# Optimization experiments

Hardware: AMD Instinct MI355X
Metric: run time of the kernel (lower is better)

Reference implementation:

```python
import jax, jax.numpy as jnp
import numpy as np

B, S, H, NH = 4, 1024, 4096, 32
QL, KVL, RD, ND, VD = 1536, 512, 64, 128, 128  # q_lora, kv_lora, rope, nope, v head dims
QHD = ND + RD  # 192
EPS = 1e-6


def setup_inputs() -> dict:
    key = jax.random.key(0)
    ks = jax.random.split(key, 10)
    def w(k, fan_in, fan_out):
        return jax.random.normal(k, (fan_in, fan_out), jnp.float32) * (fan_in ** -0.5)
    return {
        "hidden_states": jax.random.normal(ks[0], (B, S, H), jnp.float32),
        "cos": jax.random.uniform(ks[1], (S, RD), jnp.float32),
        "sin": jax.random.uniform(ks[2], (S, RD), jnp.float32),
        "position_ids": jax.random.randint(ks[3], (B, S), 0, S, jnp.int64 if jax.config.jax_enable_x64 else jnp.int32),
        "Wqa": w(ks[4], H, QL),
        "gqa": jnp.ones((QL,), jnp.float32),
        "bqa": jnp.zeros((QL,), jnp.float32),
        "Wqb": w(ks[5], QL, NH * QHD),
        "Wkva": w(ks[6], H, KVL + RD),
        "gkva": jnp.ones((KVL,), jnp.float32),
        "bkva": jnp.zeros((KVL,), jnp.float32),
        "Wkvb": w(ks[7], KVL, NH * (ND + VD)),
        "Wo": w(ks[8], NH * VD, H),
    }


def _ln(x, g, b):
    m = jnp.mean(x, -1, keepdims=True)
    v = jnp.mean(jnp.square(x - m), -1, keepdims=True)
    return (x - m) * jax.lax.rsqrt(v + EPS) * g + b


def _rotate_half(x):
    x1, x2 = jnp.split(x, 2, axis=-1)
    return jnp.concatenate([-x2, x1], axis=-1)


def _rope(t, cos_g, sin_g):
    # t: (B,S,h,RD); cos_g/sin_g: (B,S,1,RD)
    return t * cos_g + _rotate_half(t) * sin_g


def reference(hidden_states, cos, sin, position_ids, Wqa, gqa, bqa, Wqb, Wkva, gkva, bkva, Wkvb, Wo):
    hs = hidden_states
    # low-rank Q path: q_a_proj -> LN -> q_b_proj
    q = _ln(hs @ Wqa, gqa, bqa) @ Wqb                      # (B,S,NH*QHD)
    q = q.reshape(B, S, NH, QHD)
    q_nope, q_pe = q[..., :ND], q[..., ND:]                # (B,S,NH,128/64)
    # compressed KV + MQA rope key
    ckv = hs @ Wkva                                        # (B,S,KVL+RD)
    kv_c, k_pe = ckv[..., :KVL], ckv[..., KVL:]
    kv_cn = _ln(kv_c, gkva, bkva)                          # (B,S,512)
    # partial-dim RoPE on rope slices only
    cos_g = cos[position_ids][:, :, None, :]               # (B,S,1,RD)
    sin_g = sin[position_ids][:, :, None, :]
    q_pe = _rope(q_pe, cos_g, sin_g)                       # (B,S,NH,RD)
    k_pe = _rope(k_pe[:, :, None, :], cos_g, sin_g)        # (B,S,1,RD)
    # decompress latent into per-head k_nope and v
    kv = (kv_cn @ Wkvb).reshape(B, S, NH, ND + VD)
    k_nope, v = kv[..., :ND], kv[..., ND:]
    k = jnp.concatenate([k_nope, jnp.broadcast_to(k_pe, (B, S, NH, RD))], axis=-1)  # (B,S,NH,192)
    qs = jnp.concatenate([q_nope, q_pe], axis=-1)          # (B,S,NH,192)
    # causal attention
    scores = jnp.einsum('bqhd,bkhd->bhqk', qs, k) * (QHD ** -0.5)
    causal = jnp.tril(jnp.ones((S, S), bool))
    scores = jnp.where(causal, scores, jnp.finfo(scores.dtype).min)
    p = jax.nn.softmax(scores, axis=-1)                    # (B,NH,S,S)
    o = jnp.einsum('bhqk,bkhd->bqhd', p, v).reshape(B, S, NH * VD)
    return o @ Wo                                          # (B,S,H)
```

## Files before the change

kernel.cpp:

```cpp
#include <hip/hip_runtime.h>

#define B_ 4
#define S_ 1024
#define H_ 4096
#define NH_ 32
#define QHD_ 192
#define EPS_ 1e-6f

typedef __bf16 bf16x8 __attribute__((ext_vector_type(8)));
typedef float floatx4 __attribute__((ext_vector_type(4)));

__device__ __forceinline__ unsigned short f2bf(float f) {
  unsigned int u = __builtin_bit_cast(unsigned int, f);
  u += 0x7fffu + ((u >> 16) & 1u);
  return (unsigned short)(u >> 16);
}
__device__ __forceinline__ float bf2f(unsigned short s) {
  return __builtin_bit_cast(float, ((unsigned int)s) << 16);
}

__device__ __forceinline__ void gload16(const unsigned short* g, unsigned short* l) {
  __builtin_amdgcn_global_load_lds(
      (const __attribute__((address_space(1))) void*)g,
      (__attribute__((address_space(3))) void*)l, 16, 0, 0);
}

__global__ __launch_bounds__(256) void convert_kernel(
    const float* __restrict__ x, unsigned short* __restrict__ y)
{
  const int i = (blockIdx.x * 256 + threadIdx.x) * 8;
  const float4 a = *(const float4*)(x + i);
  const float4 b = *(const float4*)(x + i + 4);
  ushort4 u, v;
  u.x = f2bf(a.x); u.y = f2bf(a.y); u.z = f2bf(a.z); u.w = f2bf(a.w);
  v.x = f2bf(b.x); v.y = f2bf(b.y); v.z = f2bf(b.z); v.w = f2bf(b.w);
  *(ushort4*)(y + i) = u;
  *(ushort4*)(y + i + 4) = v;
}

__global__ __launch_bounds__(256) void transpose_kernel(
    const float* __restrict__ W, unsigned short* __restrict__ Wt,
    const int K, const int N)
{
  __shared__ float tile[32][33];
  const int tx = threadIdx.x & 31, ty = threadIdx.x >> 5;
  const int nb = blockIdx.x << 5, kb = blockIdx.y << 5;
#pragma unroll
  for (int j = 0; j < 4; ++j)
    tile[ty + j * 8][tx] = W[(size_t)(kb + ty + j * 8) * N + nb + tx];
  __syncthreads();
#pragma unroll
  for (int j = 0; j < 4; ++j)
    Wt[(size_t)(nb + ty + j * 8) * K + kb + tx] = f2bf(tile[tx][ty + j * 8]);
}

template<int OMODE>
__global__ __launch_bounds__(256, 2) void gemm_bt(
    const unsigned short* __restrict__ A, const unsigned short* __restrict__ Bt,
    void* __restrict__ Cv, const int N, const int K,
    const int lda, const int ldb, const int ldc)
{
  __shared__ unsigned short As[128 * 32];
  __shared__ unsigned short Bs[128 * 32];

  const int t = threadIdx.x;
  const int m0 = blockIdx.x * 128, n0 = blockIdx.y * 128;
  const int w = t >> 6, lane = t & 63;
  const int wm = (w >> 1) << 6, wn = (w & 1) << 6;
  const int lm = lane & 15, lq = lane >> 4;

  const floatx4 vzero = {0.f, 0.f, 0.f, 0.f};
  floatx4 acc[4][4];
#pragma unroll
  for (int i = 0; i < 4; ++i)
#pragma unroll
    for (int j = 0; j < 4; ++j) acc[i][j] = vzero;

  const int srow = (w << 5) + (lane >> 2);
  const int skc = (lane & 3) << 3;
  const unsigned short* gA = A + (size_t)(m0 + srow) * lda + skc;
  const unsigned short* gB = Bt + (size_t)(n0 + srow) * ldb + skc;
  unsigned short* lA0 = &As[(w << 1) * 512];
  unsigned short* lA1 = &As[((w << 1) + 1) * 512];
  unsigned short* lB0 = &Bs[(w << 1) * 512];
  unsigned short* lB1 = &Bs[((w << 1) + 1) * 512];

  const int nk = K >> 5;
  for (int kb = 0; kb < nk; ++kb) {
    const int k0 = kb << 5;
    __syncthreads();
    gload16(gA + k0, lA0);
    gload16(gA + (size_t)16 * lda + k0, lA1);
    gload16(gB + k0, lB0);
    gload16(gB + (size_t)16 * ldb + k0, lB1);
    __syncthreads();

    bf16x8 af[4], bfr[4];
#pragma unroll
    for (int mi = 0; mi < 4; ++mi)
      af[mi] = *(const bf16x8*)&As[(wm + mi * 16 + lm) * 32 + (lq << 3)];
#pragma unroll
    for (int ni = 0; ni < 4; ++ni)
      bfr[ni] = *(const bf16x8*)&Bs[(wn + ni * 16 + lm) * 32 + (lq << 3)];
#pragma unroll
    for (int mi = 0; mi < 4; ++mi)
#pragma unroll
      for (int ni = 0; ni < 4; ++ni)
        acc[mi][ni] = __builtin_amdgcn_mfma_f32_16x16x32_bf16(af[mi], bfr[ni], acc[mi][ni], 0, 0, 0);
  }

#pragma unroll
  for (int mi = 0; mi < 4; ++mi) {
    const int row = m0 + wm + mi * 16 + (lq << 2);
#pragma unroll
    for (int ni = 0; ni < 4; ++ni) {
      const int col = n0 + wn + ni * 16 + lm;
      if (col < N) {
#pragma unroll
        for (int r = 0; r < 4; ++r) {
          if constexpr (OMODE == 0)
            ((float*)Cv)[(size_t)(row + r) * ldc + col] = acc[mi][ni][r];
          else if constexpr (OMODE == 1)
            ((unsigned short*)Cv)[(size_t)(row + r) * ldc + col] = f2bf(acc[mi][ni][r]);
          else {
            const int rr2 = row + r;
            ((unsigned short*)Cv)[(((size_t)(rr2 >> 10) * NH_ + (col >> 8)) * S_ + (rr2 & 1023)) * 256 + (col & 255)] = f2bf(acc[mi][ni][r]);
          }
        }
      }
    }
  }
}

__global__ __launch_bounds__(256) void ln_kernel(
    const float* __restrict__ x, const float* __restrict__ g,
    const float* __restrict__ bias, unsigned short* __restrict__ y,
    const int L, const int xstride, const int ystride)
{
  __shared__ float sh[4];
  const int t = threadIdx.x;
  const float* xr = x + (size_t)blockIdx.x * xstride;
  unsigned short* yr = y + (size_t)blockIdx.x * ystride;
  const int n = L >> 8;
  float vals[6];
  float s = 0.f;
  for (int i = 0; i < n; ++i) { vals[i] = xr[t + (i << 8)]; s += vals[i]; }
#pragma unroll
  for (int off = 32; off; off >>= 1) s += __shfl_down(s, off);
  if ((t & 63) == 0) sh[t >> 6] = s;
  __syncthreads();
  const float mean = (sh[0] + sh[1] + sh[2] + sh[3]) / (float)L;
  float vs = 0.f;
  for (int i = 0; i < n; ++i) { const float d = vals[i] - mean; vs += d * d; }
#pragma unroll
  for (int off = 32; off; off >>= 1) vs += __shfl_down(vs, off);
  __syncthreads();
  if ((t & 63) == 0) sh[t >> 6] = vs;
  __syncthreads();
  const float inv = rsqrtf((sh[0] + sh[1] + sh[2] + sh[3]) / (float)L + EPS_);
  for (int i = 0; i < n; ++i) {
    const int c = t + (i << 8);
    yr[c] = f2bf((vals[i] - mean) * inv * g[c] + bias[c]);
  }
}

__global__ __launch_bounds__(256) void rope_q_kernel(
    unsigned short* __restrict__ q, const float* __restrict__ cosp,
    const float* __restrict__ sinp, const int* __restrict__ pos)
{
  const int i = blockIdx.x * 256 + threadIdx.x;
  const int p = i & 31;
  const int h = (i >> 5) & 31;
  const int bs = i >> 10;
  const int pid = pos[bs];
  const size_t base = ((size_t)bs * NH_ + h) * QHD_ + 128;
  const float x1 = bf2f(q[base + p]);
  const float x2 = bf2f(q[base + p + 32]);
  const float* cr = cosp + (size_t)pid * 64;
  const float* sr = sinp + (size_t)pid * 64;
  q[base + p]      = f2bf(x1 * cr[p] - x2 * sr[p]);
  q[base + p + 32] = f2bf(x2 * cr[p + 32] + x1 * sr[p + 32]);
}

__global__ __launch_bounds__(256) void rope_k_kernel(
    const float* __restrict__ ckv, const float* __restrict__ cosp,
    const float* __restrict__ sinp, const int* __restrict__ pos,
    unsigned short* __restrict__ kpe)
{
  const int i = blockIdx.x * 256 + threadIdx.x;
  const int p = i & 31;
  const int bs = i >> 5;
  const int pid = pos[bs];
  const float* row = ckv + (size_t)bs * 576 + 512;
  const float x1 = row[p], x2 = row[p + 32];
  const float* cr = cosp + (size_t)pid * 64;
  const float* sr = sinp + (size_t)pid * 64;
  kpe[(size_t)bs * 64 + p]      = f2bf(x1 * cr[p] - x2 * sr[p]);
  kpe[(size_t)bs * 64 + p + 32] = f2bf(x2 * cr[p + 32] + x1 * sr[p + 32]);
}

__global__ __launch_bounds__(256, 3) void attn_kernel(
    const unsigned short* __restrict__ qb, const unsigned short* __restrict__ kvb,
    const unsigned short* __restrict__ kpe, unsigned short* __restrict__ o)
{
  __shared__ unsigned short Ks[64 * 200];
  __shared__ unsigned short Vt[128 * 72];
  __shared__ unsigned short Ps[4 * 16 * 72];

  const int t = threadIdx.x;
  const int qt = (int)gridDim.x - 1 - (int)blockIdx.x;
  const int h = blockIdx.y, b = blockIdx.z;
  const int w = t >> 6, lane = t & 63;
  const int lm = lane & 15, lq = lane >> 4;
  const float SCALE2 = 0.10411754645f;

  const unsigned short* qp = qb + (((size_t)b * S_ + (qt << 6) + (w << 4) + lm) * NH_ + h) * QHD_;
  bf16x8 qf[6];
#pragma unroll
  for (int s = 0; s < 6; ++s) qf[s] = *(const bf16x8*)(qp + s * 32 + (lq << 3));

  const floatx4 vzero = {0.f, 0.f, 0.f, 0.f};
  floatx4 of[8];
#pragma unroll
  for (int i = 0; i < 8; ++i) of[i] = vzero;
  float mrow[4] = {-1e30f, -1e30f, -1e30f, -1e30f};
  float lrow[4] = {0.f, 0.f, 0.f, 0.f};

  const unsigned short* kvbase = kvb + (size_t)(b * NH_ + h) * S_ * 256;
  const unsigned short* kpbase = kpe + (size_t)b * S_ * 64;

  uint4 rKa0, rKa1, rKa2, rKa3;
  uint4 rKp0, rKp1;
  uint4 rVa0, rVb0, rVa1, rVb1;

  const int tK  = (t >> 4) * 256 + ((t & 15) << 3);
  const int tKp = (t >> 3) * 64 + ((t & 7) << 3);
  const int cg  = t & 15;
  const int tV  = ((t >> 4) << 1) * 256 + 128 + (cg << 3);

#define LOAD_TILE(KT) do { \
    const unsigned short* kvt_ = kvbase + (size_t)((KT) << 6) * 256; \
    const unsigned short* kpt_ = kpbase + (size_t)((KT) << 6) * 64;  \
    rKa0 = *(const uint4*)(kvt_ + tK);                                \
    rKa1 = *(const uint4*)(kvt_ + 16 * 256 + tK);                     \
    rKa2 = *(const uint4*)(kvt_ + 32 * 256 + tK);                     \
    rKa3 = *(const uint4*)(kvt_ + 48 * 256 + tK);                     \
    rKp0 = *(const uint4*)(kpt_ + tKp);                               \
    rKp1 = *(const uint4*)(kpt_ + 32 * 64 + tKp);                     \
    rVa0 = *(const uint4*)(kvt_ + tV);                                \
    rVb0 = *(const uint4*)(kvt_ + tV + 256);                          \
    rVa1 = *(const uint4*)(kvt_ + 32 * 256 + tV);                     \
    rVb1 = *(const uint4*)(kvt_ + 32 * 256 + tV + 256);               \
  } while (0)

#define STORE_V(VA, VB, KP) do { \
    const int sc_ = ((KP) ^ ((cg & 7) << 2)) << 1;                      \
    unsigned short* vb_ = &Vt[(cg << 3) * 72 + sc_];                    \
    *(unsigned int*)(vb_ + 0 * 72) = ((VA).x & 0xffffu) | ((VB).x << 16);        \
    *(unsigned int*)(vb_ + 1 * 72) = ((VA).x >> 16)     | ((VB).x & 0xffff0000u);\
    *(unsigned int*)(vb_ + 2 * 72) = ((VA).y & 0xffffu) | ((VB).y << 16);        \
    *(unsigned int*)(vb_ + 3 * 72) = ((VA).y >> 16)     | ((VB).y & 0xffff0000u);\
    *(unsigned int*)(vb_ + 4 * 72) = ((VA).z & 0xffffu) | ((VB).z << 16);        \
    *(unsigned int*)(vb_ + 5 * 72) = ((VA).z >> 16)     | ((VB).z & 0xffff0000u);\
    *(unsigned int*)(vb_ + 6 * 72) = ((VA).w & 0xffffu) | ((VB).w << 16);        \
    *(unsigned int*)(vb_ + 7 * 72) = ((VA).w >> 16)     | ((VB).w & 0xffff0000u);\
  } while (0)

  LOAD_TILE(0);

  const int wKs  = (t >> 4) * 200 + ((t & 15) << 3);
  const int wKps = (t >> 3) * 200 + 128 + ((t & 7) << 3);

  for (int kt = 0; kt <= qt; ++kt) {
    __syncthreads();
    *(uint4*)&Ks[wKs]            = rKa0;
    *(uint4*)&Ks[16 * 200 + wKs] = rKa1;
    *(uint4*)&Ks[32 * 200 + wKs] = rKa2;
    *(uint4*)&Ks[48 * 200 + wKs] = rKa3;
    *(uint4*)&Ks[wKps]            = rKp0;
    *(uint4*)&Ks[32 * 200 + wKps] = rKp1;
    STORE_V(rVa0, rVb0, (t >> 4));
    STORE_V(rVa1, rVb1, 16 + (t >> 4));
    __syncthreads();
    if (kt < qt) LOAD_TILE(kt + 1);

    const bool diag = (kt == qt);
    const int nimax = diag ? w : 3;

    floatx4 sacc[4];
#pragma unroll
    for (int ni = 0; ni < 4; ++ni) sacc[ni] = vzero;
    for (int ni = 0; ni <= nimax; ++ni) {
#pragma unroll
      for (int s = 0; s < 6; ++s) {
        const bf16x8 kf = *(const bf16x8*)&Ks[(ni * 16 + lm) * 200 + s * 32 + (lq << 3)];
        sacc[ni] = __builtin_amdgcn_mfma_f32_16x16x32_bf16(qf[s], kf, sacc[ni], 0, 0, 0);
      }
    }

#pragma unroll
    for (int r = 0; r < 4; ++r) {
      const int rq = (lq << 2) + r;
      float sc[4], mx = -1e30f;
#pragma unroll
      for (int ni = 0; ni < 4; ++ni) {
        float v = sacc[ni][r] * SCALE2;
        if (ni > nimax) v = -1e30f;
        if (diag && ni == w && lm > rq) v = -1e30f;
        sc[ni] = v;
        mx = fmaxf(mx, v);
      }
#pragma unroll
      for (int off = 8; off; off >>= 1) mx = fmaxf(mx, __shfl_xor(mx, off));
      const float mnew = fmaxf(mrow[r], mx);
      const float al = __builtin_amdgcn_exp2f(mrow[r] - mnew);
      mrow[r] = mnew;
      float ps = 0.f;
#pragma unroll
      for (int ni = 0; ni < 4; ++ni) {
        const float p = __builtin_amdgcn_exp2f(sc[ni] - mnew);
        ps += p;
        Ps[(w * 16 + rq) * 72 + ni * 16 + lm] = f2bf(p);
      }
#pragma unroll
      for (int off = 8; off; off >>= 1) ps += __shfl_xor(ps, off);
      lrow[r] = lrow[r] * al + ps;
#pragma unroll
      for (int vt = 0; vt < 8; ++vt) of[vt][r] *= al;
    }

    const int ksmax = diag ? ((w >= 2) ? 1 : 0) : 1;
    for (int ks2 = 0; ks2 <= ksmax; ++ks2) {
      const bf16x8 pf = *(const bf16x8*)&Ps[(w * 16 + lm) * 72 + ks2 * 32 + (lq << 3)];
#pragma unroll
      for (int vt = 0; vt < 8; ++vt) {
        const int rr = vt * 16 + lm;
        const int c0 = (ks2 << 4) + (lq << 2);
        const bf16x8 vf = *(const bf16x8*)&Vt[rr * 72 + ((c0 ^ (((rr >> 3) & 7) << 2)) << 1)];
        of[vt] = __builtin_amdgcn_mfma_f32_16x16x32_bf16(pf, vf, of[vt], 0, 0, 0);
      }
    }
  }

#pragma unroll
  for (int r = 0; r < 4; ++r) {
    const int qrow = (qt << 6) + (w << 4) + (lq << 2) + r;
    const float inv = 1.f / lrow[r];
    unsigned short* orow = o + ((size_t)b * S_ + qrow) * 4096 + h * 128;
#pragma unroll
    for (int vt = 0; vt < 8; ++vt)
      orow[vt * 16 + lm] = f2bf(of[vt][r] * inv);
  }
#undef LOAD_TILE
#undef STORE_V
}

extern "C" void kernel_launch(void* const* d_in, const int* in_sizes, int n_in,
                              void* d_out, int out_size, void* d_ws, size_t ws_size,
                              hipStream_t stream) {
  (void)in_sizes; (void)n_in; (void)out_size; (void)ws_size;
  const float* hs   = (const float*)d_in[0];
  const float* cosp = (const float*)d_in[1];
  const float* sinp = (const float*)d_in[2];
  const int*   pos  = (const int*)d_in[3];
  const float* Wqa  = (const float*)d_in[4];
  const float* gqa  = (const float*)d_in[5];
  const float* bqa  = (const float*)d_in[6];
  const float* Wqb  = (const float*)d_in[7];
  const float* Wkva = (const float*)d_in[8];
  const float* gkva = (const float*)d_in[9];
  const float* bkva = (const float*)d_in[10];
  const float* Wkvb = (const float*)d_in[11];
  const float* Wo   = (const float*)d_in[12];
  float* out = (float*)d_out;

  char* ws = (char*)d_ws;
  unsigned short* hsb   = (unsigned short*)(ws);
  float*          q_a   = (float*)(ws + 33554432);
  unsigned short* qb    = (unsigned short*)(ws);
  unsigned short* WqaT  = (unsigned short*)(ws + 58720256);
  unsigned short* WkvaT = (unsigned short*)(ws + 71303168);
  unsigned short* qln   = (unsigned short*)(ws + 58720256);
  unsigned short* kvln  = (unsigned short*)(ws + 71303168);
  unsigned short* WqbT  = (unsigned short*)(ws + 76546048);
  float*          ckv   = (float*)(ws + 95420416);
  unsigned short* WkvbT = (unsigned short*)(ws + 104857600);
  unsigned short* ob    = (unsigned short*)(ws + 76546048);
  unsigned short* WoT   = (unsigned short*)(ws + 113246208);
  unsigned short* kvb   = (unsigned short*)(ws + 146800640);
  unsigned short* kpe   = (unsigned short*)(ws + 213909504);

  const dim3 blk(256);
  convert_kernel<<<dim3(8192), blk, 0, stream>>>(hs, hsb);
  transpose_kernel<<<dim3(48, 128), blk, 0, stream>>>(Wqa, WqaT, 4096, 1536);
  transpose_kernel<<<dim3(18, 128), blk, 0, stream>>>(Wkva, WkvaT, 4096, 576);
  transpose_kernel<<<dim3(192, 48), blk, 0, stream>>>(Wqb, WqbT, 1536, 6144);
  transpose_kernel<<<dim3(256, 16), blk, 0, stream>>>(Wkvb, WkvbT, 512, 8192);
  transpose_kernel<<<dim3(128, 128), blk, 0, stream>>>(Wo, WoT, 4096, 4096);

  gemm_bt<0><<<dim3(32, 12), blk, 0, stream>>>(hsb, WqaT, q_a, 1536, 4096, 4096, 4096, 1536);
  gemm_bt<0><<<dim3(32, 5), blk, 0, stream>>>(hsb, WkvaT, ckv, 576, 4096, 4096, 4096, 576);
  ln_kernel<<<dim3(4096), blk, 0, stream>>>(q_a, gqa, bqa, qln, 1536, 1536, 1536);
  ln_kernel<<<dim3(4096), blk, 0, stream>>>(ckv, gkva, bkva, kvln, 512, 576, 512);
  rope_k_kernel<<<dim3(512), blk, 0, stream>>>(ckv, cosp, sinp, pos, kpe);
  gemm_bt<1><<<dim3(32, 48), blk, 0, stream>>>(qln, WqbT, qb, 6144, 1536, 1536, 1536, 6144);
  rope_q_kernel<<<dim3(16384), blk, 0, stream>>>(qb, cosp, sinp, pos);
  gemm_bt<2><<<dim3(32, 64), blk, 0, stream>>>(kvln, WkvbT, kvb, 8192, 512, 512, 512, 8192);
  attn_kernel<<<dim3(16, 32, 4), blk, 0, stream>>>(qb, kvb, kpe, ob);
  gemm_bt<0><<<dim3(32, 32), blk, 0, stream>>>(ob, WoT, out, 4096, 4096, 4096, 4096, 4096);
}
```

Measured before the change: 983.4 us.

## Use 128-row query tiles with 512-thread attention blocks sharing each K/V tile

The attention kernel now processes 128 query rows per block with 8 waves instead of 64 rows with 4 waves. Each K/V tile is loaded once into shared memory and reused by twice as many query rows, and the cooperative load per thread is halved. Causal masking becomes per-wave, so waves whose rows sit entirely above a key tile skip it. This halves global K/V traffic per query but produces idle waves near the diagonal and half as many blocks.

```diff
diff --git a/kernel.cpp b/kernel.cpp
--- a/kernel.cpp
+++ b/kernel.cpp
@@ -199,22 +199,22 @@
   kpe[(size_t)bs * 64 + p + 32] = f2bf(x2 * cr[p + 32] + x1 * sr[p + 32]);
 }
 
-__global__ __launch_bounds__(256, 3) void attn_kernel(
+__global__ __launch_bounds__(512, 4) void attn_kernel(
     const unsigned short* __restrict__ qb, const unsigned short* __restrict__ kvb,
     const unsigned short* __restrict__ kpe, unsigned short* __restrict__ o)
 {
   __shared__ unsigned short Ks[64 * 200];
   __shared__ unsigned short Vt[128 * 72];
-  __shared__ unsigned short Ps[4 * 16 * 72];
+  __shared__ unsigned short Ps[8 * 16 * 72];
 
   const int t = threadIdx.x;
-  const int qt = (int)gridDim.x - 1 - (int)blockIdx.x;
+  const int q0 = (int)gridDim.x - 1 - (int)blockIdx.x;
   const int h = blockIdx.y, b = blockIdx.z;
   const int w = t >> 6, lane = t & 63;
   const int lm = lane & 15, lq = lane >> 4;
   const float SCALE2 = 0.10411754645f;
 
-  const unsigned short* qp = qb + (((size_t)b * S_ + (qt << 6) + (w << 4) + lm) * NH_ + h) * QHD_;
+  const unsigned short* qp = qb + (((size_t)b * S_ + (q0 << 7) + (w << 4) + lm) * NH_ + h) * QHD_;
   bf16x8 qf[6];
 #pragma unroll
   for (int s = 0; s < 6; ++s) qf[s] = *(const bf16x8*)(qp + s * 32 + (lq << 3));
@@ -229,122 +229,134 @@
   const unsigned short* kvbase = kvb + (size_t)(b * NH_ + h) * S_ * 256;
   const unsigned short* kpbase = kpe + (size_t)b * S_ * 64;
 
-  uint4 rKa0, rKa1, rKa2, rKa3;
-  uint4 rKp0, rKp1;
-  uint4 rVa0, rVb0, rVa1, rVb1;
+  uint4 rKa0, rKa1, rKp0, rVa0, rVb0;
 
   const int tK  = (t >> 4) * 256 + ((t & 15) << 3);
   const int tKp = (t >> 3) * 64 + ((t & 7) << 3);
   const int cg  = t & 15;
-  const int tV  = ((t >> 4) << 1) * 256 + 128 + (cg << 3);
+  const int kp  = t >> 4;
+  const int tV  = (kp << 1) * 256 + 128 + (cg << 3);
 
 #define LOAD_TILE(KT) do { \
     const unsigned short* kvt_ = kvbase + (size_t)((KT) << 6) * 256; \
     const unsigned short* kpt_ = kpbase + (size_t)((KT) << 6) * 64;  \
     rKa0 = *(const uint4*)(kvt_ + tK);                                \
-    rKa1 = *(const uint4*)(kvt_ + 16 * 256 + tK);                     \
-    rKa2 = *(const uint4*)(kvt_ + 32 * 256 + tK);                     \
-    rKa3 = *(const uint4*)(kvt_ + 48 * 256 + tK);                     \
+    rKa1 = *(const uint4*)(kvt_ + 32 * 256 + tK);                     \
     rKp0 = *(const uint4*)(kpt_ + tKp);                               \
-    rKp1 = *(const uint4*)(kpt_ + 32 * 64 + tKp);                     \
     rVa0 = *(const uint4*)(kvt_ + tV);                                \
     rVb0 = *(const uint4*)(kvt_ + tV + 256);                          \
-    rVa1 = *(const uint4*)(kvt_ + 32 * 256 + tV);                     \
-    rVb1 = *(const uint4*)(kvt_ + 32 * 256 + tV + 256);               \
-  } while (0)
-
-#define STORE_V(VA, VB, KP) do { \
-    const int sc_ = ((KP) ^ ((cg & 7) << 2)) << 1;                      \
-    unsigned short* vb_ = &Vt[(cg << 3) * 72 + sc_];                    \
-    *(unsigned int*)(vb_ + 0 * 72) = ((VA).x & 0xffffu) | ((VB).x << 16);        \
-    *(unsigned int*)(vb_ + 1 * 72) = ((VA).x >> 16)     | ((VB).x & 0xffff0000u);\
-    *(unsigned int*)(vb_ + 2 * 72) = ((VA).y & 0xffffu) | ((VB).y << 16);        \
-    *(unsigned int*)(vb_ + 3 * 72) = ((VA).y >> 16)     | ((VB).y & 0xffff0000u);\
-    *(unsigned int*)(vb_ + 4 * 72) = ((VA).z & 0xffffu) | ((VB).z << 16);        \
-    *(unsigned int*)(vb_ + 5 * 72) = ((VA).z >> 16)     | ((VB).z & 0xffff0000u);\
-    *(unsigned int*)(vb_ + 6 * 72) = ((VA).w & 0xffffu) | ((VB).w << 16);        \
-    *(unsigned int*)(vb_ + 7 * 72) = ((VA).w >> 16)     | ((VB).w & 0xffff0000u);\
   } while (0)
 
   LOAD_TILE(0);
 
   const int wKs  = (t >> 4) * 200 + ((t & 15) << 3);
   const int wKps = (t >> 3) * 200 + 128 + ((t & 7) << 3);
-
-  for (int kt = 0; kt <= qt; ++kt) {
+  const int scv  = (kp ^ ((cg & 7) << 2)) << 1;
+  unsigned short* vbp = &Vt[(cg << 3) * 72 + scv];
+
+  const int ktmax = (q0 << 1) + 1;
+  const int qrel0 = (q0 << 7) + (w << 4);
+
+  for (int kt = 0; kt <= ktmax; ++kt) {
     __syncthreads();
     *(uint4*)&Ks[wKs]            = rKa0;
-    *(uint4*)&Ks[16 * 200 + wKs] = rKa1;
-    *(uint4*)&Ks[32 * 200 + wKs] = rKa2;
-    *(uint4*)&Ks[48 * 200 + wKs] = rKa3;
-    *(uint4*)&Ks[wKps]            = rKp0;
-    *(uint4*)&Ks[32 * 200 + wKps] = rKp1;
-    STORE_V(rVa0, rVb0, (t >> 4));
-    STORE_V(rVa1, rVb1, 16 + (t >> 4));
+    *(uint4*)&Ks[32 * 200 + wKs] = rKa1;
+    *(uint4*)&Ks[wKps]           = rKp0;
+    *(unsigned int*)(vbp + 0 * 72) = (rVa0.x & 0xffffu) | (rVb0.x << 16);
+    *(unsigned int*)(vbp + 1 * 72) = (rVa0.x >> 16)     | (rVb0.x & 0xffff0000u);
+    *(unsigned int*)(vbp + 2 * 72) = (rVa0.y & 0xffffu) | (rVb0.y << 16);
+    *(unsigned int*)(vbp + 3 * 72) = (rVa0.y >> 16)     | (rVb0.y & 0xffff0000u);
+    *(unsigned int*)(vbp + 4 * 72) = (rVa0.z & 0xffffu) | (rVb0.z << 16);
+    *(unsigned int*)(vbp + 5 * 72) = (rVa0.z >> 16)     | (rVb0.z & 0xffff0000u);
+    *(unsigned int*)(vbp + 6 * 72) = (rVa0.w & 0xffffu) | (rVb0.w << 16);
+    *(unsigned int*)(vbp + 7 * 72) = (rVa0.w >> 16)     | (rVb0.w & 0xffff0000u);
     __syncthreads();
-    if (kt < qt) LOAD_TILE(kt + 1);
-
-    const bool diag = (kt == qt);
-    const int nimax = diag ? w : 3;
-
-    floatx4 sacc[4];
-#pragma unroll
-    for (int ni = 0; ni < 4; ++ni) sacc[ni] = vzero;
-    for (int ni = 0; ni <= nimax; ++ni) {
-#pragma unroll
-      for (int s = 0; s < 6; ++s) {
-        const bf16x8 kf = *(const bf16x8*)&Ks[(ni * 16 + lm) * 200 + s * 32 + (lq << 3)];
-        sacc[ni] = __builtin_amdgcn_mfma_f32_16x16x32_bf16(qf[s], kf, sacc[ni], 0, 0, 0);
+    if (kt < ktmax) LOAD_TILE(kt + 1);
+
+    const int rel = qrel0 - (kt << 6);
+    if (rel >= 0) {
+      const int nimax = (rel >= 64) ? 3 : (rel >> 4);
+
+      floatx4 s0v = vzero, s1v = vzero, s2v = vzero, s3v = vzero;
+#define QKNI(SACC, NI) do { \
+      _Pragma("unroll") \
+      for (int s = 0; s < 6; ++s) { \
+        const bf16x8 kf = *(const bf16x8*)&Ks[((NI) * 16 + lm) * 200 + s * 32 + (lq << 3)]; \
+        SACC = __builtin_amdgcn_mfma_f32_16x16x32_bf16(qf[s], kf, SACC, 0, 0, 0); \
+      } } while (0)
+      QKNI(s0v, 0);
+      if (nimax >= 1) QKNI(s1v, 1);
+      if (nimax >= 2) QKNI(s2v, 2);
+      if (nimax >= 3) QKNI(s3v, 3);
+#undef QKNI
+
+      const bool dg = (rel < 64);
+#pragma unroll
+      for (int r = 0; r < 4; ++r) {
+        const int rq = (lq << 2) + r;
+        float a0 = s0v[r] * SCALE2;
+        float a1 = s1v[r] * SCALE2;
+        float a2 = s2v[r] * SCALE2;
+        float a3 = s3v[r] * SCALE2;
+        if (nimax < 1) a1 = -1e30f;
+        if (nimax < 2) a2 = -1e30f;
+        if (nimax < 3) a3 = -1e30f;
+        if (dg) {
+          const bool m = lm > rq;
+          if (nimax == 0 && m) a0 = -1e30f;
+          if (nimax == 1 && m) a1 = -1e30f;
+          if (nimax == 2 && m) a2 = -1e30f;
+          if (nimax == 3 && m) a3 = -1e30f;
+        }
+        float mx = fmaxf(fmaxf(a0, a1), fmaxf(a2, a3));
+#pragma unroll
+        for (int off = 8; off; off >>= 1) mx = fmaxf(mx, __shfl_xor(mx, off));
+        const float mnew = fmaxf(mrow[r], mx);
+        const float al = __builtin_amdgcn_exp2f(mrow[r] - mnew);
+        mrow[r] = mnew;
+        const float p0 = __builtin_amdgcn_exp2f(a0 - mnew);
+        const float p1 = __builtin_amdgcn_exp2f(a1 - mnew);
+        const float p2 = __builtin_amdgcn_exp2f(a2 - mnew);
+        const float p3 = __builtin_amdgcn_exp2f(a3 - mnew);
+        unsigned short* pr = &Ps[(w * 16 + rq) * 72 + lm];
+        pr[0]  = f2bf(p0);
+        pr[16] = f2bf(p1);
+        pr[32] = f2bf(p2);
+        pr[48] = f2bf(p3);
+        float ps = (p0 + p1) + (p2 + p3);
+#pragma unroll
+        for (int off = 8; off; off >>= 1) ps += __shfl_xor(ps, off);
+        lrow[r] = lrow[r] * al + ps;
+#pragma unroll
+        for (int vt = 0; vt < 8; ++vt) of[vt][r] *= al;
       }
-    }
-
-#pragma unroll
-    for (int r = 0; r < 4; ++r) {
-      const int rq = (lq << 2) + r;
-      float sc[4], mx = -1e30f;
-#pragma unroll
-      for (int ni = 0; ni < 4; ++ni) {
-        float v = sacc[ni][r] * SCALE2;
-        if (ni > nimax) v = -1e30f;
-        if (diag && ni == w && lm > rq) v = -1e30f;
-        sc[ni] = v;
-        mx = fmaxf(mx, v);
+
+      {
+        const bf16x8 pf = *(const bf16x8*)&Ps[(w * 16 + lm) * 72 + (lq << 3)];
+#pragma unroll
+        for (int vt = 0; vt < 8; ++vt) {
+          const int rr = vt * 16 + lm;
+          const int c0 = (lq << 2);
+          const bf16x8 vf = *(const bf16x8*)&Vt[rr * 72 + ((c0 ^ (((rr >> 3) & 7) << 2)) << 1)];
+          of[vt] = __builtin_amdgcn_mfma_f32_16x16x32_bf16(pf, vf, of[vt], 0, 0, 0);
+        }
       }
-#pragma unroll
-      for (int off = 8; off; off >>= 1) mx = fmaxf(mx, __shfl_xor(mx, off));
-      const float mnew = fmaxf(mrow[r], mx);
-      const float al = __builtin_amdgcn_exp2f(mrow[r] - mnew);
-      mrow[r] = mnew;
-      float ps = 0.f;
-#pragma unroll
-      for (int ni = 0; ni < 4; ++ni) {
-        const float p = __builtin_amdgcn_exp2f(sc[ni] - mnew);
-        ps += p;
-        Ps[(w * 16 + rq) * 72 + ni * 16 + lm] = f2bf(p);
-      }
-#pragma unroll
-      for (int off = 8; off; off >>= 1) ps += __shfl_xor(ps, off);
-      lrow[r] = lrow[r] * al + ps;
-#pragma unroll
-      for (int vt = 0; vt < 8; ++vt) of[vt][r] *= al;
-    }
-
-    const int ksmax = diag ? ((w >= 2) ? 1 : 0) : 1;
-    for (int ks2 = 0; ks2 <= ksmax; ++ks2) {
-      const bf16x8 pf = *(const bf16x8*)&Ps[(w * 16 + lm) * 72 + ks2 * 32 + (lq << 3)];
-#pragma unroll
-      for (int vt = 0; vt < 8; ++vt) {
-        const int rr = vt * 16 + lm;
-        const int c0 = (ks2 << 4) + (lq << 2);
-        const bf16x8 vf = *(const bf16x8*)&Vt[rr * 72 + ((c0 ^ (((rr >> 3) & 7) << 2)) << 1)];
-        of[vt] = __builtin_amdgcn_mfma_f32_16x16x32_bf16(pf, vf, of[vt], 0, 0, 0);
+      if (rel >= 32) {
+        const bf16x8 pf = *(const bf16x8*)&Ps[(w * 16 + lm) * 72 + 32 + (lq << 3)];
+#pragma unroll
+        for (int vt = 0; vt < 8; ++vt) {
+          const int rr = vt * 16 + lm;
+          const int c0 = 16 + (lq << 2);
+          const bf16x8 vf = *(const bf16x8*)&Vt[rr * 72 + ((c0 ^ (((rr >> 3) & 7) << 2)) << 1)];
+          of[vt] = __builtin_amdgcn_mfma_f32_16x16x32_bf16(pf, vf, of[vt], 0, 0, 0);
+        }
       }
     }
   }
 
 #pragma unroll
   for (int r = 0; r < 4; ++r) {
-    const int qrow = (qt << 6) + (w << 4) + (lq << 2) + r;
+    const int qrow = (q0 << 7) + (w << 4) + (lq << 2) + r;
     const float inv = 1.f / lrow[r];
     unsigned short* orow = o + ((size_t)b * S_ + qrow) * 4096 + h * 128;
 #pragma unroll
@@ -352,7 +364,6 @@
       orow[vt * 16 + lm] = f2bf(of[vt][r] * inv);
   }
 #undef LOAD_TILE
-#undef STORE_V
 }
 
 extern "C" void kernel_launch(void* const* d_in, const int* in_sizes, int n_in,
@@ -406,6 +417,6 @@
   gemm_bt<1><<<dim3(32, 48), blk, 0, stream>>>(qln, WqbT, qb, 6144, 1536, 1536, 1536, 6144);
   rope_q_kernel<<<dim3(16384), blk, 0, stream>>>(qb, cosp, sinp, pos);
   gemm_bt<2><<<dim3(32, 64), blk, 0, stream>>>(kvln, WkvbT, kvb, 8192, 512, 512, 512, 8192);
-  attn_kernel<<<dim3(16, 32, 4), blk, 0, stream>>>(qb, kvb, kpe, ob);
+  attn_kernel<<<dim3(8, 32, 4), dim3(512), 0, stream>>>(qb, kvb, kpe, ob);
   gemm_bt<0><<<dim3(32, 32), blk, 0, stream>>>(ob, WoT, out, 4096, 4096, 4096, 4096, 4096);
 }
```

Measured after the change: 983.3 us. No clear change (-0.0%).
